# Performance work log

Measured on AMD Instinct MI355X. Metric: run time of the kernel, lower is better.

Reference implementation:

```python
import jax, jax.numpy as jnp
import numpy as np

B, T, C, H = 4, 1024, 1024, 16
D = C // H  # head dim = 64
EPS = 1e-5


def _layernorm(x, g, b):
    m = jnp.mean(x, axis=-1, keepdims=True)
    v = jnp.var(x, axis=-1, keepdims=True)
    return (x - m) / jnp.sqrt(v + EPS) * g + b


def setup_inputs() -> dict:
    key = jax.random.key(0)
    ks = jax.random.split(key, 8)
    s = 0.02  # GPT-style init scale
    w = lambda k, shp: (jax.random.normal(k, shp, jnp.float32) * s)
    return {
        "x": jax.random.normal(ks[0], (B, T, C), jnp.float32),
        "ln1_g": jnp.ones((C,), jnp.float32), "ln1_b": jnp.zeros((C,), jnp.float32),
        "wq": w(ks[1], (C, C)), "bq": jnp.zeros((C,), jnp.float32),
        "wk": w(ks[2], (C, C)), "bk": jnp.zeros((C,), jnp.float32),
        "wv": w(ks[3], (C, C)), "bv": jnp.zeros((C,), jnp.float32),
        "wo": w(ks[4], (C, C)), "bo": jnp.zeros((C,), jnp.float32),
        "ln2_g": jnp.ones((C,), jnp.float32), "ln2_b": jnp.zeros((C,), jnp.float32),
        "w1": w(ks[5], (C, 4 * C)), "b1": jnp.zeros((4 * C,), jnp.float32),
        "w2": w(ks[6], (4 * C, C)), "b2": jnp.zeros((C,), jnp.float32),
    }


def reference(x, ln1_g, ln1_b, wq, bq, wk, bk, wv, bv, wo, bo,
              ln2_g, ln2_b, w1, b1, w2, b2):
    # --- causal self-attention branch: x = x + attn(ln1(x)) ---
    h = _layernorm(x, ln1_g, ln1_b)
    q = (h @ wq + bq).reshape(B, T, H, D)
    k = (h @ wk + bk).reshape(B, T, H, D)
    v = (h @ wv + bv).reshape(B, T, H, D)
    att = jnp.einsum('bqhd,bkhd->bhqk', q, k) * (1.0 / np.sqrt(D).astype(np.float32))
    causal = jnp.tril(jnp.ones((T, T), bool))
    att = jnp.where(causal, att, -jnp.inf)
    att = jax.nn.softmax(att, axis=-1)  # dropout p=0 -> identity
    y = jnp.einsum('bhqk,bkhd->bqhd', att, v).reshape(B, T, C)
    x = x + (y @ wo + bo)
    # --- MLP branch: x = x + mlp(ln2(x)) ---
    h2 = _layernorm(x, ln2_g, ln2_b)
    m = jax.nn.gelu(h2 @ w1 + b1, approximate=False)  # torch nn.GELU default = exact erf
    x = x + (m @ w2 + b2)
    return x
```

## Files before the change

kernel.cpp:

```cpp
#include <hip/hip_runtime.h>
#include <hip/hip_bf16.h>
#include <math.h>

#define B_ 4
#define T_ 1024
#define C_ 1024
#define H_ 16
#define D_ 64
#define M_ (B_*T_)

typedef __bf16 bf16;
typedef __bf16 bf16x8 __attribute__((ext_vector_type(8)));
typedef float  f32x4  __attribute__((ext_vector_type(4)));

#define MFMA16(a, b, c) __builtin_amdgcn_mfma_f32_16x16x32_bf16((a), (b), (c), 0, 0, 0)

__device__ __forceinline__ void gload16(const void* g, void* l) {
  __builtin_amdgcn_global_load_lds((const __attribute__((address_space(1))) void*)g,
                                   (__attribute__((address_space(3))) void*)l,
                                   16, 0, 0);
}

__global__ __launch_bounds__(256) void prep_k(
    const float* __restrict__ x, const float* __restrict__ ln1g,
    const float* __restrict__ ln1b,
    const float* __restrict__ wq, const float* __restrict__ wk,
    const float* __restrict__ wv, const float* __restrict__ wo,
    const float* __restrict__ w1, const float* __restrict__ w2,
    const float* __restrict__ bq, const float* __restrict__ bk,
    const float* __restrict__ bv,
    bf16* __restrict__ WqkvT, bf16* __restrict__ WoT,
    bf16* __restrict__ W1T, bf16* __restrict__ W2T,
    bf16* __restrict__ hbuf, float* __restrict__ bqkv) {
  __shared__ float tile[64][65];
  const int blk = blockIdx.x, tid = threadIdx.x;
  if (blk < 3072) {
    const float* W; bf16* WT; int K, N, n0, k0;
    if (blk < 1024)      { const int w = blk >> 8, t = blk & 255;
                           W  = (w == 0) ? wq : (w == 1) ? wk : (w == 2) ? wv : wo;
                           WT = (w < 3) ? WqkvT + (size_t)w * 1024 * 1024 : WoT;
                           K = 1024; N = 1024; n0 = (t & 15) * 64; k0 = (t >> 4) * 64; }
    else if (blk < 2048) { const int t = blk - 1024; W = w1; WT = W1T;
                           K = 1024; N = 4096; n0 = (t & 63) * 64; k0 = (t >> 6) * 64; }
    else                 { const int t = blk - 2048; W = w2; WT = W2T;
                           K = 4096; N = 1024; n0 = (t & 15) * 64; k0 = (t >> 4) * 64; }
    const int tr = tid >> 4, tc4 = (tid & 15) * 4;
#pragma unroll
    for (int p = 0; p < 4; ++p) {
      float4 v = *(const float4*)(W + (size_t)(k0 + tr + p * 16) * N + n0 + tc4);
      tile[tr + p * 16][tc4]     = v.x;
      tile[tr + p * 16][tc4 + 1] = v.y;
      tile[tr + p * 16][tc4 + 2] = v.z;
      tile[tr + p * 16][tc4 + 3] = v.w;
    }
    __syncthreads();
    const int nr = tid >> 3, k8 = (tid & 7) * 8;
#pragma unroll
    for (int p = 0; p < 2; ++p) {
      const int n = nr + p * 32;
      bf16x8 o8;
#pragma unroll
      for (int j = 0; j < 8; ++j) o8[j] = (bf16)tile[k8 + j][n];
      *(bf16x8*)(WT + (size_t)(n0 + n) * K + k0 + k8) = o8;
    }
  } else if (blk < 7168) {
    const int row = blk - 3072;
    float4 xv = ((const float4*)(x + (size_t)row * C_))[tid];
    float s  = xv.x + xv.y + xv.z + xv.w;
    float ss = xv.x*xv.x + xv.y*xv.y + xv.z*xv.z + xv.w*xv.w;
#pragma unroll
    for (int m = 32; m; m >>= 1) { s += __shfl_xor(s, m); ss += __shfl_xor(ss, m); }
    float* red = &tile[0][0];
    const int wid = tid >> 6;
    if ((tid & 63) == 0) { red[wid] = s; red[4 + wid] = ss; }
    __syncthreads();
    s  = red[0] + red[1] + red[2] + red[3];
    ss = red[4] + red[5] + red[6] + red[7];
    const float mean = s * (1.0f / C_);
    const float var  = ss * (1.0f / C_) - mean * mean;
    const float inv  = rsqrtf(var + 1e-5f);
    float4 gv = ((const float4*)ln1g)[tid];
    float4 bv = ((const float4*)ln1b)[tid];
    bf16* o = hbuf + (size_t)row * C_ + tid * 4;
    o[0] = (bf16)((xv.x - mean) * inv * gv.x + bv.x);
    o[1] = (bf16)((xv.y - mean) * inv * gv.y + bv.y);
    o[2] = (bf16)((xv.z - mean) * inv * gv.z + bv.z);
    o[3] = (bf16)((xv.w - mean) * inv * gv.w + bv.w);
  } else {
    const int i = (blk - 7168) * 256 + tid;
    bqkv[i] = (i < 1024) ? bq[i] : ((i < 2048) ? bk[i - 1024] : bv[i - 2048]);
  }
}

__global__ __launch_bounds__(256) void ln_k(const float* __restrict__ x,
                                            const float* __restrict__ g,
                                            const float* __restrict__ b,
                                            bf16* __restrict__ out) {
  int row = blockIdx.x;
  int t = threadIdx.x;
  float4 xv = ((const float4*)(x + (size_t)row * C_))[t];
  float s  = xv.x + xv.y + xv.z + xv.w;
  float ss = xv.x*xv.x + xv.y*xv.y + xv.z*xv.z + xv.w*xv.w;
#pragma unroll
  for (int m = 32; m; m >>= 1) { s += __shfl_xor(s, m); ss += __shfl_xor(ss, m); }
  __shared__ float red[8];
  int wid = t >> 6;
  if ((t & 63) == 0) { red[wid] = s; red[4 + wid] = ss; }
  __syncthreads();
  s  = red[0] + red[1] + red[2] + red[3];
  ss = red[4] + red[5] + red[6] + red[7];
  float mean = s * (1.0f / C_);
  float var  = ss * (1.0f / C_) - mean * mean;
  float inv  = rsqrtf(var + 1e-5f);
  float4 gv = ((const float4*)g)[t];
  float4 bv = ((const float4*)b)[t];
  bf16* o = out + (size_t)row * C_ + t * 4;
  o[0] = (bf16)((xv.x - mean) * inv * gv.x + bv.x);
  o[1] = (bf16)((xv.y - mean) * inv * gv.y + bv.y);
  o[2] = (bf16)((xv.z - mean) * inv * gv.z + bv.z);
  o[3] = (bf16)((xv.w - mean) * inv * gv.w + bv.w);
}

template <int BM, int BN, int WM, int WN, int EPI>
__global__ __launch_bounds__(WM*WN*64, 4)
void gemms(const bf16* __restrict__ A, const bf16* __restrict__ BT,
           const float* __restrict__ bias, const float* __restrict__ res,
           void* __restrict__ outp, int N, int K, int gx) {
  constexpr int NT = WM * WN * 64;
  constexpr int FM = BM / WM / 16, FN = BN / WN / 16;
  constexpr int RA = BM / 32, RB = BN / 32;
  __shared__ __align__(16) bf16 smem[(BM + BN) * 64];
  bf16* sA = smem;
  bf16* sB = smem + BM * 64;
  const int tid = threadIdx.x, lane = tid & 63, wid = tid >> 6;
  const int wr = wid / WN, wc = wid % WN;

  int bid = blockIdx.x;
  const int nwg = gridDim.x;
  if (!(nwg & 7)) bid = (bid & 7) * (nwg >> 3) + (bid >> 3);
  const int bx = bid % gx, by = bid / gx;
  const size_t am0 = (size_t)bx * BM, bn0 = (size_t)by * BN;

  f32x4 acc[FM][FN];
  const f32x4 fz = {0.f, 0.f, 0.f, 0.f};
#pragma unroll
  for (int m = 0; m < FM; ++m)
#pragma unroll
    for (int n = 0; n < FN; ++n) acc[m][n] = fz;

  const int srow = tid >> 3;
  const int sg = (tid & 7) ^ (srow & 7);
  const bf16* ag = A  + (am0 + srow) * (size_t)K + sg * 8;
  const bf16* bg = BT + (bn0 + srow) * (size_t)K + sg * 8;

  const int arow = lane & 15;
  const int g0 = (((lane >> 4))     ^ (lane & 7)) * 8;
  const int g1 = (((lane >> 4) + 4) ^ (lane & 7)) * 8;
  const int nt = K >> 6;

#pragma unroll
  for (int r = 0; r < RA; ++r)
    gload16(ag + (size_t)(r * 32) * K, sA + r * 2048 + tid * 8);
#pragma unroll
  for (int r = 0; r < RB; ++r)
    gload16(bg + (size_t)(r * 32) * K, sB + r * 2048 + tid * 8);

  for (int t = 0; t < nt; ++t) {
    __syncthreads();

    const bf16* pa = sA + (wr * (BM / WM) + arow) * 64;
    const bf16* pb = sB + (wc * (BN / WN) + arow) * 64;
    bf16x8 a[FM], b[FN];
#pragma unroll
    for (int m = 0; m < FM; ++m) a[m] = *(const bf16x8*)(pa + m * 16 * 64 + g0);
#pragma unroll
    for (int n = 0; n < FN; ++n) b[n] = *(const bf16x8*)(pb + n * 16 * 64 + g0);
#pragma unroll
    for (int m = 0; m < FM; ++m)
#pragma unroll
      for (int n = 0; n < FN; ++n)
        acc[m][n] = MFMA16(a[m], b[n], acc[m][n]);
    bf16x8 a1[FM], b1[FN];
#pragma unroll
    for (int m = 0; m < FM; ++m) a1[m] = *(const bf16x8*)(pa + m * 16 * 64 + g1);
#pragma unroll
    for (int n = 0; n < FN; ++n) b1[n] = *(const bf16x8*)(pb + n * 16 * 64 + g1);

    __syncthreads();

    if (t + 1 < nt) {
#pragma unroll
      for (int r = 0; r < RA; ++r)
        gload16(ag + (size_t)(t + 1) * 64 + (size_t)(r * 32) * K,
                sA + r * 2048 + tid * 8);
#pragma unroll
      for (int r = 0; r < RB; ++r)
        gload16(bg + (size_t)(t + 1) * 64 + (size_t)(r * 32) * K,
                sB + r * 2048 + tid * 8);
    }
#pragma unroll
    for (int m = 0; m < FM; ++m)
#pragma unroll
      for (int n = 0; n < FN; ++n)
        acc[m][n] = MFMA16(a1[m], b1[n], acc[m][n]);
  }

  if constexpr (EPI != 2) {
#pragma unroll
    for (int m = 0; m < FM; ++m) {
      const int row0 = wr * (BM / WM) + m * 16 + (lane >> 4) * 4;
#pragma unroll
      for (int n = 0; n < FN; ++n) {
        const int col = wc * (BN / WN) + n * 16 + (lane & 15);
        const float bv = bias[bn0 + col];
#pragma unroll
        for (int j = 0; j < 4; ++j) {
          float v = acc[m][n][j] + bv;
          if constexpr (EPI == 1) v = 0.5f * v * (1.0f + erff(v * 0.70710678118f));
          const int rr = row0 + j;
          smem[rr * BN + (((col >> 3) ^ (rr & 7)) << 3) + (col & 7)] = (bf16)v;
        }
      }
    }
    __syncthreads();
    constexpr int GR = BN / 8;
    constexpr int SI = BM * BN / (NT * 8);
#pragma unroll
    for (int i = 0; i < SI; ++i) {
      const int idx = i * NT + tid;
      const int row = idx / GR, g = idx % GR;
      *(bf16x8*)((bf16*)outp + (am0 + row) * N + bn0 + g * 8) =
          *(const bf16x8*)(smem + row * BN + ((g ^ (row & 7)) << 3));
    }
  } else {
    constexpr int PR = BM / WM;
    float* sf = (float*)smem;
#pragma unroll
    for (int h = 0; h < WM; ++h) {
      __syncthreads();
      if (wr == h) {
#pragma unroll
        for (int m = 0; m < FM; ++m) {
          const int lr0 = m * 16 + (lane >> 4) * 4;
#pragma unroll
          for (int n = 0; n < FN; ++n) {
            const int col = wc * (BN / WN) + n * 16 + (lane & 15);
            const float bv = bias[bn0 + col];
#pragma unroll
            for (int j = 0; j < 4; ++j)
              sf[(lr0 + j) * BN + col] = acc[m][n][j] + bv;
          }
        }
      }
      __syncthreads();
      constexpr int SI = PR * BN / (NT * 4);
#pragma unroll
      for (int i = 0; i < SI; ++i) {
        const int flat = (i * NT + tid) * 4;
        const int row = flat / BN, c = flat % BN;
        const size_t gi = (am0 + h * PR + row) * N + bn0 + c;
        float4 rv = *(const float4*)(res + gi);
        float4 sv = *(const float4*)(sf + row * BN + c);
        rv.x += sv.x; rv.y += sv.y; rv.z += sv.z; rv.w += sv.w;
        *(float4*)((float*)outp + gi) = rv;
      }
    }
  }
}

__global__ __launch_bounds__(256, 4) void attn_k(const bf16* __restrict__ Q,
                                                 const bf16* __restrict__ Kb,
                                                 const bf16* __restrict__ Vb,
                                                 bf16* __restrict__ Y, int ld) {
  const int bh = blockIdx.x;
  const int b = bh >> 4, h = bh & 15;
  const int u = (int)gridDim.y - 1 - (int)blockIdx.y;
  const int q0 = u * 128;
  const int tid = threadIdx.x, wid = tid >> 6, lane = tid & 63;

  __shared__ __align__(16) bf16 sK[2][64 * 64];
  __shared__ __align__(16) bf16 sVT[2][64 * 64];
  __shared__ __align__(16) bf16 sP[4][16 * 64];

  const size_t rowQ0 = (size_t)(b * T_ + q0 + wid * 16 + (lane & 15)) * ld + h * 64 + (lane >> 4) * 8;
  const bf16x8 qaf0 = *(const bf16x8*)(Q + rowQ0);
  const bf16x8 qaf1 = *(const bf16x8*)(Q + rowQ0 + 32);
  const size_t rowQ1 = rowQ0 + (size_t)64 * ld;
  const bf16x8 qbf0 = *(const bf16x8*)(Q + rowQ1);
  const bf16x8 qbf1 = *(const bf16x8*)(Q + rowQ1 + 32);

  const f32x4 fz = {0.f, 0.f, 0.f, 0.f};
  float mA[4] = {-1e30f, -1e30f, -1e30f, -1e30f}, lA[4] = {0.f, 0.f, 0.f, 0.f};
  float mB[4] = {-1e30f, -1e30f, -1e30f, -1e30f}, lB[4] = {0.f, 0.f, 0.f, 0.f};
  f32x4 oA[4], oB[4];
#pragma unroll
  for (int i = 0; i < 4; ++i) { oA[i] = fz; oB[i] = fz; }

  const int kgr = (lane & 7) ^ (lane >> 3);
  const bf16* kg = Kb + (size_t)(b * T_ + wid * 16 + (lane >> 3)) * ld + h * 64 + kgr * 8;
  const int lkoff = (wid * 16) * 64;
  const bf16* vg = Vb + (size_t)(b * T_ + lane) * ld + h * 64;

  const int g0 = (((lane >> 4))     ^ (lane & 7)) * 8;
  const int g1 = (((lane >> 4) + 4) ^ (lane & 7)) * 8;

  gload16(kg,                   sK[0] + lkoff);
  gload16(kg + (size_t)8 * ld,  sK[0] + lkoff + 8 * 64);
  {
    bf16x8 v0 = *(const bf16x8*)(vg + wid * 8);
    bf16x8 v1 = *(const bf16x8*)(vg + (wid + 4) * 8);
#pragma unroll
    for (int j = 0; j < 8; ++j) {
      const int pc = ((((lane >> 3) ^ j) << 3) | (lane & 7));
      sVT[0][(wid * 8 + j) * 64 + pc]       = v0[j];
      sVT[0][((wid + 4) * 8 + j) * 64 + pc] = v1[j];
    }
  }

  const int ktmax = 2 * u + 1;
  int k0 = 0, cur = 0;

  auto subtile = [&](const bf16x8& qf0, const bf16x8& qf1, int rbase,
                     float* m_run, float* l_run, f32x4* o) {
    f32x4 s[4];
#pragma unroll
    for (int ni = 0; ni < 4; ++ni) {
      const bf16* kr = sK[cur] + (ni * 16 + (lane & 15)) * 64;
      bf16x8 kf0 = *(const bf16x8*)(kr + g0);
      bf16x8 kf1 = *(const bf16x8*)(kr + g1);
      f32x4 t = fz;
      t = MFMA16(qf0, kf0, t);
      t = MFMA16(qf1, kf1, t);
      s[ni] = t;
    }
    const int cbase = k0 + (lane & 15);
    float tm[4] = {-1e30f, -1e30f, -1e30f, -1e30f};
#pragma unroll
    for (int ni = 0; ni < 4; ++ni)
#pragma unroll
      for (int j = 0; j < 4; ++j) {
        float v = s[ni][j] * 0.125f;
        if (cbase + ni * 16 > rbase + j) v = -1e30f;
        s[ni][j] = v;
        tm[j] = fmaxf(tm[j], v);
      }
#pragma unroll
    for (int j = 0; j < 4; ++j)
#pragma unroll
      for (int mk = 1; mk < 16; mk <<= 1)
        tm[j] = fmaxf(tm[j], __shfl_xor(tm[j], mk));

    float fac[4], rs[4] = {0.f, 0.f, 0.f, 0.f};
#pragma unroll
    for (int j = 0; j < 4; ++j) {
      float mn = fmaxf(m_run[j], tm[j]);
      fac[j] = __expf(m_run[j] - mn);
      m_run[j] = mn;
    }
#pragma unroll
    for (int ni = 0; ni < 4; ++ni)
#pragma unroll
      for (int j = 0; j < 4; ++j) {
        float p = __expf(s[ni][j] - m_run[j]);
        rs[j] += p;
        const int crow = (lane >> 4) * 4 + j;
        const int cg = (ni * 2 + ((lane & 15) >> 3)) ^ (crow & 7);
        sP[wid][crow * 64 + (cg << 3) + (lane & 7)] = (bf16)p;
      }
#pragma unroll
    for (int j = 0; j < 4; ++j) {
#pragma unroll
      for (int mk = 1; mk < 16; mk <<= 1)
        rs[j] += __shfl_xor(rs[j], mk);
      l_run[j] = l_run[j] * fac[j] + rs[j];
    }
#pragma unroll
    for (int df = 0; df < 4; ++df)
#pragma unroll
      for (int j = 0; j < 4; ++j)
        o[df][j] *= fac[j];
#pragma unroll
    for (int kk = 0; kk < 2; ++kk) {
      const int gk = kk ? g1 : g0;
      bf16x8 pf8 = *(const bf16x8*)(sP[wid] + (lane & 15) * 64 + gk);
#pragma unroll
      for (int df = 0; df < 4; ++df) {
        bf16x8 vf = *(const bf16x8*)(sVT[cur] + (df * 16 + (lane & 15)) * 64 + gk);
        o[df] = MFMA16(pf8, vf, o[df]);
      }
    }
  };

  for (int kt = 0; kt <= ktmax; ++kt) {
    cur = kt & 1;
    const int nxt = cur ^ 1;
    const bool pf = (kt < ktmax);
    __syncthreads();

    bf16x8 vn0, vn1;
    if (pf) {
      const size_t k1 = (size_t)(kt + 1) * 64;
      gload16(kg + k1 * ld,        sK[nxt] + lkoff);
      gload16(kg + (k1 + 8) * ld,  sK[nxt] + lkoff + 8 * 64);
      vn0 = *(const bf16x8*)(vg + k1 * ld + wid * 8);
      vn1 = *(const bf16x8*)(vg + k1 * ld + (wid + 4) * 8);
    }

    k0 = kt * 64;
    const int rb = q0 + wid * 16 + (lane >> 4) * 4;
    if (kt < ktmax)
      subtile(qaf0, qaf1, rb,      mA, lA, oA);
    subtile(qbf0, qbf1, rb + 64,   mB, lB, oB);

    if (pf) {
#pragma unroll
      for (int j = 0; j < 8; ++j) {
        const int pc = ((((lane >> 3) ^ j) << 3) | (lane & 7));
        sVT[nxt][(wid * 8 + j) * 64 + pc]       = vn0[j];
        sVT[nxt][((wid + 4) * 8 + j) * 64 + pc] = vn1[j];
      }
    }
  }

#pragma unroll
  for (int df = 0; df < 4; ++df)
#pragma unroll
    for (int j = 0; j < 4; ++j) {
      const int row = q0 + wid * 16 + (lane >> 4) * 4 + j;
      const int d = df * 16 + (lane & 15);
      Y[(size_t)(b * T_ + row) * C_ + h * 64 + d]      = (bf16)(oA[df][j] / lA[j]);
      Y[(size_t)(b * T_ + row + 64) * C_ + h * 64 + d] = (bf16)(oB[df][j] / lB[j]);
    }
}

extern "C" void kernel_launch(void* const* d_in, const int* in_sizes, int n_in,
                              void* d_out, int out_size, void* d_ws, size_t ws_size,
                              hipStream_t stream) {
  (void)in_sizes; (void)n_in; (void)out_size; (void)ws_size;
  const float* x    = (const float*)d_in[0];
  const float* ln1g = (const float*)d_in[1];
  const float* ln1b = (const float*)d_in[2];
  const float* wq   = (const float*)d_in[3];
  const float* bq   = (const float*)d_in[4];
  const float* wk   = (const float*)d_in[5];
  const float* bk   = (const float*)d_in[6];
  const float* wv   = (const float*)d_in[7];
  const float* bv   = (const float*)d_in[8];
  const float* wo   = (const float*)d_in[9];
  const float* bo   = (const float*)d_in[10];
  const float* ln2g = (const float*)d_in[11];
  const float* ln2b = (const float*)d_in[12];
  const float* w1   = (const float*)d_in[13];
  const float* b1   = (const float*)d_in[14];
  const float* w2   = (const float*)d_in[15];
  const float* b2   = (const float*)d_in[16];

  char* ws = (char*)d_ws;
  const size_t MB = 1024 * 1024;
  bf16* WqkvT = (bf16*)(ws +  0 * MB);
  bf16* WoT   = (bf16*)(ws +  6 * MB);
  bf16* W1T   = (bf16*)(ws +  8 * MB);
  bf16* W2T   = (bf16*)(ws + 16 * MB);
  bf16* hbuf  = (bf16*)(ws + 24 * MB);
  bf16* qkv   = (bf16*)(ws + 32 * MB);
  bf16* yb    = (bf16*)(ws + 56 * MB);
  bf16* mb    = (bf16*)(ws + 32 * MB);
  float* x1   = (float*)(ws + 64 * MB);
  float* bqkv = (float*)d_out;

  dim3 blk(256);
  prep_k<<<7180, blk, 0, stream>>>(x, ln1g, ln1b, wq, wk, wv, wo, w1, w2,
                                   bq, bk, bv, WqkvT, WoT, W1T, W2T, hbuf, bqkv);
  gemms<128,128,2,2,0><<<768,  blk, 0, stream>>>(hbuf, WqkvT, bqkv, nullptr, qkv, 3072, 1024, 32);
  attn_k<<<dim3(64, 8), blk, 0, stream>>>(qkv, qkv + 1024, qkv + 2048, yb, 3072);
  gemms<64,128,2,2,2><<<512,   blk, 0, stream>>>(yb, WoT, bo, x, x1, 1024, 1024, 64);
  ln_k<<<M_, blk, 0, stream>>>(x1, ln2g, ln2b, hbuf);
  gemms<128,128,2,2,1><<<1024, blk, 0, stream>>>(hbuf, W1T, b1, nullptr, mb, 4096, 1024, 32);
  gemms<64,128,2,2,2><<<512,   blk, 0, stream>>>(mb, W2T, b2, x1, (float*)d_out, 1024, 4096, 64);
}
```

Before: 261.5 us.

## Shrink attention query tile to 64 rows per block and double grid

Attention blocks now process a single 64-row query tile instead of two 64-row subtiles sharing each K/V tile, and the grid doubles along the query dimension. This removes the per-block two-subtile structure and gives more, smaller blocks for load balancing. In exchange each K/V tile is loaded and transposed into shared memory twice as often overall, and the occupancy hint in launch bounds is dropped.

```diff
diff --git a/kernel.cpp b/kernel.cpp
--- a/kernel.cpp
+++ b/kernel.cpp
@@ -268,33 +268,30 @@
   }
 }
 
-__global__ __launch_bounds__(256, 4) void attn_k(const bf16* __restrict__ Q,
-                                                 const bf16* __restrict__ Kb,
-                                                 const bf16* __restrict__ Vb,
-                                                 bf16* __restrict__ Y, int ld) {
-  const int bh = blockIdx.x;
-  const int b = bh >> 4, h = bh & 15;
-  const int u = (int)gridDim.y - 1 - (int)blockIdx.y;
-  const int q0 = u * 128;
-  const int tid = threadIdx.x, wid = tid >> 6, lane = tid & 63;
+__global__ __launch_bounds__(256) void attn_k(const bf16* __restrict__ Q,
+                                              const bf16* __restrict__ Kb,
+                                              const bf16* __restrict__ Vb,
+                                              bf16* __restrict__ Y, int ld) {
+  int bh = blockIdx.x;
+  int b = bh >> 4, h = bh & 15;
+  int qt = (int)gridDim.y - 1 - (int)blockIdx.y;
+  int q0 = qt * 64;
+  int tid = threadIdx.x, wid = tid >> 6, lane = tid & 63;
 
   __shared__ __align__(16) bf16 sK[2][64 * 64];
   __shared__ __align__(16) bf16 sVT[2][64 * 64];
   __shared__ __align__(16) bf16 sP[4][16 * 64];
 
-  const size_t rowQ0 = (size_t)(b * T_ + q0 + wid * 16 + (lane & 15)) * ld + h * 64 + (lane >> 4) * 8;
-  const bf16x8 qaf0 = *(const bf16x8*)(Q + rowQ0);
-  const bf16x8 qaf1 = *(const bf16x8*)(Q + rowQ0 + 32);
-  const size_t rowQ1 = rowQ0 + (size_t)64 * ld;
-  const bf16x8 qbf0 = *(const bf16x8*)(Q + rowQ1);
-  const bf16x8 qbf1 = *(const bf16x8*)(Q + rowQ1 + 32);
-
+  const size_t rowQ = (size_t)(b * T_ + q0 + wid * 16 + (lane & 15)) * ld + h * 64 + (lane >> 4) * 8;
+  bf16x8 qf0 = *(const bf16x8*)(Q + rowQ);
+  bf16x8 qf1 = *(const bf16x8*)(Q + rowQ + 32);
+
+  float m_run[4] = {-1e30f, -1e30f, -1e30f, -1e30f};
+  float l_run[4] = {0.f, 0.f, 0.f, 0.f};
   const f32x4 fz = {0.f, 0.f, 0.f, 0.f};
-  float mA[4] = {-1e30f, -1e30f, -1e30f, -1e30f}, lA[4] = {0.f, 0.f, 0.f, 0.f};
-  float mB[4] = {-1e30f, -1e30f, -1e30f, -1e30f}, lB[4] = {0.f, 0.f, 0.f, 0.f};
-  f32x4 oA[4], oB[4];
-#pragma unroll
-  for (int i = 0; i < 4; ++i) { oA[i] = fz; oB[i] = fz; }
+  f32x4 o[4];
+#pragma unroll
+  for (int i = 0; i < 4; ++i) o[i] = fz;
 
   const int kgr = (lane & 7) ^ (lane >> 3);
   const bf16* kg = Kb + (size_t)(b * T_ + wid * 16 + (lane >> 3)) * ld + h * 64 + kgr * 8;
@@ -317,11 +314,21 @@
     }
   }
 
-  const int ktmax = 2 * u + 1;
-  int k0 = 0, cur = 0;
-
-  auto subtile = [&](const bf16x8& qf0, const bf16x8& qf1, int rbase,
-                     float* m_run, float* l_run, f32x4* o) {
+  for (int kt = 0; kt <= qt; ++kt) {
+    const int cur = kt & 1, nxt = cur ^ 1;
+    const bool pf = (kt < qt);
+    __syncthreads();
+
+    bf16x8 vn0, vn1;
+    if (pf) {
+      const size_t k1 = (size_t)(kt + 1) * 64;
+      gload16(kg + k1 * ld,        sK[nxt] + lkoff);
+      gload16(kg + (k1 + 8) * ld,  sK[nxt] + lkoff + 8 * 64);
+      vn0 = *(const bf16x8*)(vg + k1 * ld + wid * 8);
+      vn1 = *(const bf16x8*)(vg + k1 * ld + (wid + 4) * 8);
+    }
+
+    const int k0 = kt * 64;
     f32x4 s[4];
 #pragma unroll
     for (int ni = 0; ni < 4; ++ni) {
@@ -333,7 +340,9 @@
       t = MFMA16(qf1, kf1, t);
       s[ni] = t;
     }
-    const int cbase = k0 + (lane & 15);
+
+    int rbase = q0 + wid * 16 + (lane >> 4) * 4;
+    int cbase = k0 + (lane & 15);
     float tm[4] = {-1e30f, -1e30f, -1e30f, -1e30f};
 #pragma unroll
     for (int ni = 0; ni < 4; ++ni)
@@ -379,6 +388,7 @@
 #pragma unroll
       for (int j = 0; j < 4; ++j)
         o[df][j] *= fac[j];
+
 #pragma unroll
     for (int kk = 0; kk < 2; ++kk) {
       const int gk = kk ? g1 : g0;
@@ -389,28 +399,6 @@
         o[df] = MFMA16(pf8, vf, o[df]);
       }
     }
-  };
-
-  for (int kt = 0; kt <= ktmax; ++kt) {
-    cur = kt & 1;
-    const int nxt = cur ^ 1;
-    const bool pf = (kt < ktmax);
-    __syncthreads();
-
-    bf16x8 vn0, vn1;
-    if (pf) {
-      const size_t k1 = (size_t)(kt + 1) * 64;
-      gload16(kg + k1 * ld,        sK[nxt] + lkoff);
-      gload16(kg + (k1 + 8) * ld,  sK[nxt] + lkoff + 8 * 64);
-      vn0 = *(const bf16x8*)(vg + k1 * ld + wid * 8);
-      vn1 = *(const bf16x8*)(vg + k1 * ld + (wid + 4) * 8);
-    }
-
-    k0 = kt * 64;
-    const int rb = q0 + wid * 16 + (lane >> 4) * 4;
-    if (kt < ktmax)
-      subtile(qaf0, qaf1, rb,      mA, lA, oA);
-    subtile(qbf0, qbf1, rb + 64,   mB, lB, oB);
 
     if (pf) {
 #pragma unroll
@@ -426,10 +414,9 @@
   for (int df = 0; df < 4; ++df)
 #pragma unroll
     for (int j = 0; j < 4; ++j) {
-      const int row = q0 + wid * 16 + (lane >> 4) * 4 + j;
-      const int d = df * 16 + (lane & 15);
-      Y[(size_t)(b * T_ + row) * C_ + h * 64 + d]      = (bf16)(oA[df][j] / lA[j]);
-      Y[(size_t)(b * T_ + row + 64) * C_ + h * 64 + d] = (bf16)(oB[df][j] / lB[j]);
+      int row = q0 + wid * 16 + (lane >> 4) * 4 + j;
+      int d = df * 16 + (lane & 15);
+      Y[(size_t)(b * T_ + row) * C_ + h * 64 + d] = (bf16)(o[df][j] / l_run[j]);
     }
 }
 
@@ -472,7 +459,7 @@
   prep_k<<<7180, blk, 0, stream>>>(x, ln1g, ln1b, wq, wk, wv, wo, w1, w2,
                                    bq, bk, bv, WqkvT, WoT, W1T, W2T, hbuf, bqkv);
   gemms<128,128,2,2,0><<<768,  blk, 0, stream>>>(hbuf, WqkvT, bqkv, nullptr, qkv, 3072, 1024, 32);
-  attn_k<<<dim3(64, 8), blk, 0, stream>>>(qkv, qkv + 1024, qkv + 2048, yb, 3072);
+  attn_k<<<dim3(64, 16), blk, 0, stream>>>(qkv, qkv + 1024, qkv + 2048, yb, 3072);
   gemms<64,128,2,2,2><<<512,   blk, 0, stream>>>(yb, WoT, bo, x, x1, 1024, 1024, 64);
   ln_k<<<M_, blk, 0, stream>>>(x1, ln2g, ln2b, hbuf);
   gemms<128,128,2,2,1><<<1024, blk, 0, stream>>>(hbuf, W1T, b1, nullptr, mb, 4096, 1024, 32);
```

Result: faster. 211.3 us (median of 4 runs) (-19.2%).
